# Kernel tuning notes

Measured on AMD Instinct MI355X. Metric: run time of the kernel, lower is better.

Reference implementation:

```python
import jax, jax.numpy as jnp
import numpy as np

N_BAND = 5  # module hardcodes self.n = 5 -> keeps |i-j| <= N_BAND-1 = 4


def setup_inputs() -> dict:
    key = jax.random.key(0)
    ks = jax.random.split(key, 6)
    B, L, H = 4, 2048, 1024
    s = 1.0 / np.sqrt(H)
    return {
        "q": jax.random.normal(ks[0], (B, L, H), jnp.float32),
        "k": jax.random.normal(ks[1], (B, L, H), jnp.float32),
        "Wq": jax.random.normal(ks[2], (H, H), jnp.float32) * s,
        "bq": jax.random.normal(ks[3], (H,), jnp.float32) * s,
        "Wk": jax.random.normal(ks[4], (H, H), jnp.float32) * s,
        "bk": jax.random.normal(ks[5], (H,), jnp.float32) * s,
    }


def reference(q, k, Wq, bq, Wk, bk):
    b, l, e = q.shape
    # nn.Linear: y = x @ W^T + b
    qs = jnp.einsum("ble,he->blh", q, Wq) + bq
    ks = jnp.einsum("ble,he->blh", k, Wk) + bk
    # dense QK^T logits, [b, l, l]
    logits = jnp.einsum("blh,bmh->blm", qs, ks)
    # banded mask: the torch loop zeroes offsets 0..n-1 on both sides -> |i-j| <= n-1
    idx = jnp.arange(l)
    band = jnp.abs(idx[:, None] - idx[None, :]) <= (N_BAND - 1)  # [l, l]
    neg_inf = jnp.array(-jnp.inf, dtype=logits.dtype)
    logits = jnp.where(band[None, :, :], logits, neg_inf)
    # every row contains its diagonal, so softmax is well-defined
    return jax.nn.softmax(logits, axis=-1)
```

## Files before the change

kernel.cpp:

```cpp
#include <hip/hip_runtime.h>
#include <math.h>

#define LSEQ 2048
#define HDIM 1024
#define BATCH 4
#define ROWS (BATCH * LSEQ)
#define NBAND 9

typedef __attribute__((ext_vector_type(8))) short bf16x8;
typedef __attribute__((ext_vector_type(4))) float f32x4;
typedef __attribute__((ext_vector_type(8))) unsigned short u16x8;

#define AS3 __attribute__((address_space(3)))
#define AS1 __attribute__((address_space(1)))

__device__ __forceinline__ void gload16(const void* gp, void* lp) {
    __builtin_amdgcn_global_load_lds((AS1 const unsigned*)gp, (AS3 unsigned*)lp, 16, 0, 0);
}

__device__ __forceinline__ unsigned short f2bf(float x) {
    unsigned u = __float_as_uint(x);
    u += 0x7FFFu + ((u >> 16) & 1u);
    return (unsigned short)(u >> 16);
}
__device__ __forceinline__ float bf2f(unsigned short h) {
    return __uint_as_float(((unsigned)h) << 16);
}

__device__ __forceinline__ void split8(float4 a, float4 b, bf16x8& hi, bf16x8& lo) {
    float v[8] = {a.x, a.y, a.z, a.w, b.x, b.y, b.z, b.w};
#pragma unroll
    for (int j = 0; j < 8; j++) {
        unsigned short h = f2bf(v[j]);
        hi[j] = (short)h;
        lo[j] = (short)f2bf(v[j] - bf2f(h));
    }
}

__global__ __launch_bounds__(256) void wpart_kernel(const float* __restrict__ Wk,
                                                    const float* __restrict__ bq,
                                                    float* __restrict__ wpart) {
    const int b = blockIdx.x;
    const int c0 = threadIdx.x * 4;
    float4 acc = {0.f, 0.f, 0.f, 0.f};
#pragma unroll
    for (int hh = 0; hh < 16; hh++) {
        const int h = b * 16 + hh;
        const float s = bq[h];
        float4 v = *reinterpret_cast<const float4*>(&Wk[(size_t)h * HDIM + c0]);
        acc.x += v.x * s; acc.y += v.y * s; acc.z += v.z * s; acc.w += v.w * s;
    }
    *reinterpret_cast<float4*>(&wpart[(size_t)b * HDIM + c0]) = acc;
}

__global__ __launch_bounds__(256) void wreduce(const float* __restrict__ wpart,
                                               float* __restrict__ w) {
    const int c = blockIdx.x * 256 + threadIdx.x;
    float s = 0.f;
#pragma unroll
    for (int b = 0; b < 64; b++) s += wpart[(size_t)b * HDIM + c];
    w[c] = s;
}

__global__ __launch_bounds__(256) void transpose_convert(const float* __restrict__ Wq,
                                                         const float* __restrict__ Wk,
                                                         unsigned short* __restrict__ qhi,
                                                         unsigned short* __restrict__ qlo,
                                                         unsigned short* __restrict__ khi,
                                                         unsigned short* __restrict__ klo) {
    __shared__ float tile[64][65];
    const int z = blockIdx.z;
    const float* src = z ? Wk : Wq;
    unsigned short* dh = z ? khi : qhi;
    unsigned short* dl = z ? klo : qlo;
    const int n0 = blockIdx.x * 64;
    const int h0 = blockIdx.y * 64;
    const int tid = threadIdx.x;

#pragma unroll
    for (int p = 0; p < 4; p++) {
        const int h = p * 16 + (tid >> 4);
        const int n = (tid & 15) * 4;
        float4 v = *reinterpret_cast<const float4*>(&src[(size_t)(h0 + h) * HDIM + n0 + n]);
        tile[h][n + 0] = v.x; tile[h][n + 1] = v.y; tile[h][n + 2] = v.z; tile[h][n + 3] = v.w;
    }
    __syncthreads();
#pragma unroll
    for (int p = 0; p < 2; p++) {
        const int n = p * 32 + (tid >> 3);
        const int h = (tid & 7) * 8;
        u16x8 hv, lv;
#pragma unroll
        for (int j = 0; j < 8; j++) {
            float x = tile[h + j][n];
            unsigned short hb = f2bf(x);
            hv[j] = hb;
            lv[j] = f2bf(x - bf2f(hb));
        }
        *reinterpret_cast<u16x8*>(&dh[(size_t)(n0 + n) * HDIM + h0 + h]) = hv;
        *reinterpret_cast<u16x8*>(&dl[(size_t)(n0 + n) * HDIM + h0 + h]) = lv;
    }
}

__global__ __launch_bounds__(256) void convert_k_beta(const float* __restrict__ k,
                                                      const float* __restrict__ w,
                                                      unsigned short* __restrict__ Xhi,
                                                      unsigned short* __restrict__ Xlo,
                                                      float* __restrict__ beta) {
    __shared__ float red[4];
    const int r = blockIdx.x;
    const int t = threadIdx.x;
    float4 v = *reinterpret_cast<const float4*>(&k[(size_t)r * HDIM + t * 4]);
    float4 wv = *reinterpret_cast<const float4*>(&w[t * 4]);
    ushort4 h, l;
    h.x = f2bf(v.x); l.x = f2bf(v.x - bf2f(h.x));
    h.y = f2bf(v.y); l.y = f2bf(v.y - bf2f(h.y));
    h.z = f2bf(v.z); l.z = f2bf(v.z - bf2f(h.z));
    h.w = f2bf(v.w); l.w = f2bf(v.w - bf2f(h.w));
    reinterpret_cast<ushort4*>(Xhi)[(size_t)r * 256 + t] = h;
    reinterpret_cast<ushort4*>(Xlo)[(size_t)r * 256 + t] = l;
    float d = v.x * wv.x + v.y * wv.y + v.z * wv.z + v.w * wv.w;
#pragma unroll
    for (int off = 32; off > 0; off >>= 1) d += __shfl_xor(d, off, 64);
    if ((t & 63) == 0) red[t >> 6] = d;
    __syncthreads();
    if (t == 0) beta[r] = red[0] + red[1] + red[2] + red[3];
}

__global__ __launch_bounds__(256, 2) void gemm_part(
        const unsigned short* __restrict__ Ahi, const unsigned short* __restrict__ Alo,
        const unsigned short* __restrict__ Bhi, const unsigned short* __restrict__ Blo,
        float* __restrict__ Cparts) {
    __shared__ unsigned short sh[4 * 4096];
    const int AHI = 0, ALO = 4096, BHI = 8192, BLO = 12288;
    const int tid = threadIdx.x;
    const int w = tid >> 6, l = tid & 63;
    const int wr = w >> 1, wc = w & 1;
    const int row0 = blockIdx.x * 128, col0 = blockIdx.y * 128;
    const int kbeg = blockIdx.z * 256;
    float* C = Cparts + (size_t)blockIdx.z * HDIM * HDIM;
    const int srow0 = (l >> 2), scbp = l & 3;

    f32x4 acc[4][4];
#pragma unroll
    for (int m = 0; m < 4; m++)
#pragma unroll
        for (int n = 0; n < 4; n++) acc[m][n] = (f32x4){0.f, 0.f, 0.f, 0.f};

    const int fr_a[4] = {wr * 64 + (l & 15), wr * 64 + 16 + (l & 15),
                         wr * 64 + 32 + (l & 15), wr * 64 + 48 + (l & 15)};
    const int fr_b[4] = {wc * 64 + (l & 15), wc * 64 + 16 + (l & 15),
                         wc * 64 + 32 + (l & 15), wc * 64 + 48 + (l & 15)};
    const int cb = l >> 4;

    for (int k0 = kbeg; k0 < kbeg + 256; k0 += 32) {
#pragma unroll
        for (int i = 0; i < 2; i++) {
            const int seg = i * 4 + w;
            const int row = seg * 16 + srow0;
            const int cbs = scbp ^ ((row >> 1) & 3);
            gload16(Ahi + (size_t)(row0 + row) * HDIM + k0 + cbs * 8, &sh[AHI + seg * 512]);
            gload16(Alo + (size_t)(row0 + row) * HDIM + k0 + cbs * 8, &sh[ALO + seg * 512]);
            gload16(Bhi + (size_t)(col0 + row) * HDIM + k0 + cbs * 8, &sh[BHI + seg * 512]);
            gload16(Blo + (size_t)(col0 + row) * HDIM + k0 + cbs * 8, &sh[BLO + seg * 512]);
        }
        __syncthreads();

        bf16x8 ah[4], al[4], bh[4], bl[4];
#pragma unroll
        for (int m = 0; m < 4; m++) {
            const int r = fr_a[m];
            const int cbs = cb ^ ((r >> 1) & 3);
            ah[m] = *reinterpret_cast<const bf16x8*>(&sh[AHI + r * 32 + cbs * 8]);
            al[m] = *reinterpret_cast<const bf16x8*>(&sh[ALO + r * 32 + cbs * 8]);
        }
#pragma unroll
        for (int n = 0; n < 4; n++) {
            const int r = fr_b[n];
            const int cbs = cb ^ ((r >> 1) & 3);
            bh[n] = *reinterpret_cast<const bf16x8*>(&sh[BHI + r * 32 + cbs * 8]);
            bl[n] = *reinterpret_cast<const bf16x8*>(&sh[BLO + r * 32 + cbs * 8]);
        }
#pragma unroll
        for (int m = 0; m < 4; m++)
#pragma unroll
            for (int n = 0; n < 4; n++) {
                acc[m][n] = __builtin_amdgcn_mfma_f32_16x16x32_bf16(ah[m], bh[n], acc[m][n], 0, 0, 0);
                acc[m][n] = __builtin_amdgcn_mfma_f32_16x16x32_bf16(ah[m], bl[n], acc[m][n], 0, 0, 0);
                acc[m][n] = __builtin_amdgcn_mfma_f32_16x16x32_bf16(al[m], bh[n], acc[m][n], 0, 0, 0);
            }
        __syncthreads();
    }

    const int lcol = l & 15, lrow = (l >> 4) * 4;
#pragma unroll
    for (int n = 0; n < 4; n++) {
        const int colg = col0 + wc * 64 + n * 16 + lcol;
#pragma unroll
        for (int m = 0; m < 4; m++) {
            const int rowg = row0 + wr * 64 + m * 16 + lrow;
#pragma unroll
            for (int v = 0; v < 4; v++)
                C[(size_t)(rowg + v) * HDIM + colg] = acc[m][n][v];
        }
    }
}

__global__ __launch_bounds__(256) void reduceM_convert(const float* __restrict__ Mparts,
                                                       unsigned short* __restrict__ Mhi,
                                                       unsigned short* __restrict__ Mlo) {
    const int idx4 = blockIdx.x * 256 + threadIdx.x;
    float4 s = {0.f, 0.f, 0.f, 0.f};
#pragma unroll
    for (int z = 0; z < 4; z++) {
        float4 v = reinterpret_cast<const float4*>(Mparts + (size_t)z * HDIM * HDIM)[idx4];
        s.x += v.x; s.y += v.y; s.z += v.z; s.w += v.w;
    }
    ushort4 h, l;
    h.x = f2bf(s.x); l.x = f2bf(s.x - bf2f(h.x));
    h.y = f2bf(s.y); l.y = f2bf(s.y - bf2f(h.y));
    h.z = f2bf(s.z); l.z = f2bf(s.z - bf2f(h.z));
    h.w = f2bf(s.w); l.w = f2bf(s.w - bf2f(h.w));
    reinterpret_cast<ushort4*>(Mhi)[idx4] = h;
    reinterpret_cast<ushort4*>(Mlo)[idx4] = l;
}

__global__ __launch_bounds__(256, 2) void gemm_t(
        const unsigned short* __restrict__ Ahi, const unsigned short* __restrict__ Alo,
        const unsigned short* __restrict__ Bhi, const unsigned short* __restrict__ Blo,
        float* __restrict__ C) {
    __shared__ unsigned short sh[4 * 4096];
    const int AHI = 0, ALO = 4096, BHI = 8192, BLO = 12288;
    const int tid = threadIdx.x;
    const int w = tid >> 6, l = tid & 63;
    const int wr = w >> 1, wc = w & 1;

    const int bid = blockIdx.y * gridDim.x + blockIdx.x;
    const int swz = (bid & 7) * 64 + (bid >> 3);
    const int row0 = (swz & 63) * 128;
    const int col0 = (swz >> 6) * 128;
    const int srow0 = (l >> 2), scbp = l & 3;

    f32x4 acc[4][4];
#pragma unroll
    for (int m = 0; m < 4; m++)
#pragma unroll
        for (int n = 0; n < 4; n++) acc[m][n] = (f32x4){0.f, 0.f, 0.f, 0.f};

    const int fr_a[4] = {wr * 64 + (l & 15), wr * 64 + 16 + (l & 15),
                         wr * 64 + 32 + (l & 15), wr * 64 + 48 + (l & 15)};
    const int fr_b[4] = {wc * 64 + (l & 15), wc * 64 + 16 + (l & 15),
                         wc * 64 + 32 + (l & 15), wc * 64 + 48 + (l & 15)};
    const int cb = l >> 4;

    for (int k0 = 0; k0 < HDIM; k0 += 32) {
#pragma unroll
        for (int i = 0; i < 2; i++) {
            const int seg = i * 4 + w;
            const int row = seg * 16 + srow0;
            const int cbs = scbp ^ ((row >> 1) & 3);
            gload16(Ahi + (size_t)(row0 + row) * HDIM + k0 + cbs * 8, &sh[AHI + seg * 512]);
            gload16(Alo + (size_t)(row0 + row) * HDIM + k0 + cbs * 8, &sh[ALO + seg * 512]);
            gload16(Bhi + (size_t)(col0 + row) * HDIM + k0 + cbs * 8, &sh[BHI + seg * 512]);
            gload16(Blo + (size_t)(col0 + row) * HDIM + k0 + cbs * 8, &sh[BLO + seg * 512]);
        }
        __syncthreads();

        bf16x8 ah[4], al[4], bh[4], bl[4];
#pragma unroll
        for (int m = 0; m < 4; m++) {
            const int r = fr_a[m];
            const int cbs = cb ^ ((r >> 1) & 3);
            ah[m] = *reinterpret_cast<const bf16x8*>(&sh[AHI + r * 32 + cbs * 8]);
            al[m] = *reinterpret_cast<const bf16x8*>(&sh[ALO + r * 32 + cbs * 8]);
        }
#pragma unroll
        for (int n = 0; n < 4; n++) {
            const int r = fr_b[n];
            const int cbs = cb ^ ((r >> 1) & 3);
            bh[n] = *reinterpret_cast<const bf16x8*>(&sh[BHI + r * 32 + cbs * 8]);
            bl[n] = *reinterpret_cast<const bf16x8*>(&sh[BLO + r * 32 + cbs * 8]);
        }
#pragma unroll
        for (int m = 0; m < 4; m++)
#pragma unroll
            for (int n = 0; n < 4; n++) {
                acc[m][n] = __builtin_amdgcn_mfma_f32_16x16x32_bf16(ah[m], bh[n], acc[m][n], 0, 0, 0);
                acc[m][n] = __builtin_amdgcn_mfma_f32_16x16x32_bf16(ah[m], bl[n], acc[m][n], 0, 0, 0);
                acc[m][n] = __builtin_amdgcn_mfma_f32_16x16x32_bf16(al[m], bh[n], acc[m][n], 0, 0, 0);
            }
        __syncthreads();
    }

    const int lcol = l & 15, lrow = (l >> 4) * 4;
#pragma unroll
    for (int n = 0; n < 4; n++) {
        const int colg = col0 + wc * 64 + n * 16 + lcol;
#pragma unroll
        for (int m = 0; m < 4; m++) {
            const int rowg = row0 + wr * 64 + m * 16 + lrow;
#pragma unroll
            for (int v = 0; v < 4; v++)
                C[(size_t)(rowg + v) * HDIM + colg] = acc[m][n][v];
        }
    }
}

__global__ __launch_bounds__(256) void band_mfma(const float* __restrict__ q,
                                                 const float* __restrict__ t,
                                                 const float* __restrict__ beta,
                                                 float* __restrict__ band) {
    __shared__ float lds_c[4][16][33];
    const int tid = threadIdx.x;
    const int w = tid >> 6, l = tid & 63;
    const int r0 = blockIdx.x * 16;
    const int b = r0 >> 11;
    const int i0 = r0 & (LSEQ - 1);
    const int fr = l & 15;
    const int kb = (l >> 4) * 8;

    const float* qrow = q + (size_t)(r0 + fr) * HDIM;
    const float* tbase = t + (size_t)b * LSEQ * HDIM;

    const int j0 = i0 - 4 + fr;
    const int j1 = i0 + 12 + fr;
    const int j0c = min(max(j0, 0), LSEQ - 1);
    const int j1c = min(max(j1, 0), LSEQ - 1);
    const bool v0 = (j0 >= 0) && (j0 < LSEQ);
    const bool v1 = (j1 >= 0) && (j1 < LSEQ);
    const bool interior = (i0 >= 4) && (i0 + 19 < LSEQ);
    const float4 fz = {0.f, 0.f, 0.f, 0.f};

    f32x4 c0 = {0.f, 0.f, 0.f, 0.f};
    f32x4 c1 = {0.f, 0.f, 0.f, 0.f};

#pragma unroll 2
    for (int ks = 0; ks < 8; ks++) {
        const int k0 = w * 256 + ks * 32 + kb;
        float4 qa = *reinterpret_cast<const float4*>(qrow + k0);
        float4 qb = *reinterpret_cast<const float4*>(qrow + k0 + 4);
        float4 t0a = *reinterpret_cast<const float4*>(tbase + (size_t)j0c * HDIM + k0);
        float4 t0b = *reinterpret_cast<const float4*>(tbase + (size_t)j0c * HDIM + k0 + 4);
        float4 t1a = *reinterpret_cast<const float4*>(tbase + (size_t)j1c * HDIM + k0);
        float4 t1b = *reinterpret_cast<const float4*>(tbase + (size_t)j1c * HDIM + k0 + 4);
        if (!interior) {
            if (!v0) { t0a = fz; t0b = fz; }
            if (!v1) { t1a = fz; t1b = fz; }
        }
        bf16x8 ah, al, b0h, b0l, b1h, b1l;
        split8(qa, qb, ah, al);
        split8(t0a, t0b, b0h, b0l);
        split8(t1a, t1b, b1h, b1l);
        c0 = __builtin_amdgcn_mfma_f32_16x16x32_bf16(ah, b0h, c0, 0, 0, 0);
        c0 = __builtin_amdgcn_mfma_f32_16x16x32_bf16(ah, b0l, c0, 0, 0, 0);
        c0 = __builtin_amdgcn_mfma_f32_16x16x32_bf16(al, b0h, c0, 0, 0, 0);
        c1 = __builtin_amdgcn_mfma_f32_16x16x32_bf16(ah, b1h, c1, 0, 0, 0);
        c1 = __builtin_amdgcn_mfma_f32_16x16x32_bf16(ah, b1l, c1, 0, 0, 0);
        c1 = __builtin_amdgcn_mfma_f32_16x16x32_bf16(al, b1h, c1, 0, 0, 0);
    }

#pragma unroll
    for (int v = 0; v < 4; v++) {
        lds_c[w][(l >> 4) * 4 + v][fr] = c0[v];
        lds_c[w][(l >> 4) * 4 + v][16 + fr] = c1[v];
    }
    __syncthreads();

#pragma unroll
    for (int e = tid; e < 512; e += 256) {
        const int rr = e >> 5, cc = e & 31;
        lds_c[0][rr][cc] = lds_c[0][rr][cc] + lds_c[1][rr][cc] +
                           lds_c[2][rr][cc] + lds_c[3][rr][cc];
    }
    __syncthreads();

    if (tid < 16) {
        const int il = i0 + tid;
        const int ig = r0 + tid;
        float lg[NBAND];
#pragma unroll
        for (int d = 0; d < NBAND; d++) {
            const int j = il + d - 4;
            lg[d] = (j >= 0 && j < LSEQ)
                    ? lds_c[0][tid][tid + d] + beta[(size_t)b * LSEQ + j]
                    : -1e30f;
        }
        float m = -1e30f;
#pragma unroll
        for (int d = 0; d < NBAND; d++) m = fmaxf(m, lg[d]);
        float p[NBAND], s = 0.f;
#pragma unroll
        for (int d = 0; d < NBAND; d++) { p[d] = expf(lg[d] - m); s += p[d]; }
        const float inv = 1.f / s;
#pragma unroll
        for (int d = 0; d < NBAND; d++) band[(size_t)ig * NBAND + d] = p[d] * inv;
    }
}

__global__ __launch_bounds__(256) void expand_band(const float* __restrict__ band,
                                                   float* __restrict__ out) {
    const size_t idx4 = (size_t)blockIdx.x * 256 + threadIdx.x;
    const size_t flat = idx4 * 4;
    const int j0 = (int)(flat & (LSEQ - 1));
    const size_t row = flat >> 11;
    const int i = (int)(row & (LSEQ - 1));
    float v[4];
#pragma unroll
    for (int s = 0; s < 4; s++) {
        const int dj = (j0 + s) - i + 4;
        v[s] = (dj >= 0 && dj < NBAND) ? band[row * NBAND + dj] : 0.f;
    }
    float4 o = {v[0], v[1], v[2], v[3]};
    *reinterpret_cast<float4*>(&out[flat]) = o;
}

__global__ __launch_bounds__(256) void gemm_nt_bias(const float* __restrict__ A,
                                                    const float* __restrict__ B,
                                                    const float* __restrict__ bias,
                                                    float* __restrict__ C) {
    __shared__ float As[8][132];
    __shared__ float Bs[8][132];
    const int tid = threadIdx.x;
    const int row0 = blockIdx.x * 128, col0 = blockIdx.y * 128;
    const int lr = tid >> 1, lc = (tid & 1) * 4;
    const int tx = tid & 15, ty = tid >> 4;
    float acc[2][2][4][4];
#pragma unroll
    for (int a = 0; a < 2; a++)
#pragma unroll
        for (int b = 0; b < 2; b++)
#pragma unroll
            for (int c = 0; c < 4; c++)
#pragma unroll
                for (int d = 0; d < 4; d++) acc[a][b][c][d] = 0.f;
    for (int k0 = 0; k0 < HDIM; k0 += 8) {
        float4 av = *reinterpret_cast<const float4*>(&A[(size_t)(row0 + lr) * HDIM + k0 + lc]);
        float4 bv = *reinterpret_cast<const float4*>(&B[(size_t)(col0 + lr) * HDIM + k0 + lc]);
        __syncthreads();
        As[lc + 0][lr] = av.x; As[lc + 1][lr] = av.y; As[lc + 2][lr] = av.z; As[lc + 3][lr] = av.w;
        Bs[lc + 0][lr] = bv.x; Bs[lc + 1][lr] = bv.y; Bs[lc + 2][lr] = bv.z; Bs[lc + 3][lr] = bv.w;
        __syncthreads();
#pragma unroll
        for (int kk = 0; kk < 8; kk++) {
            float4 a0 = *reinterpret_cast<const float4*>(&As[kk][ty * 4]);
            float4 a1 = *reinterpret_cast<const float4*>(&As[kk][64 + ty * 4]);
            float4 b0 = *reinterpret_cast<const float4*>(&Bs[kk][tx * 4]);
            float4 b1 = *reinterpret_cast<const float4*>(&Bs[kk][64 + tx * 4]);
            float am[2][4] = {{a0.x, a0.y, a0.z, a0.w}, {a1.x, a1.y, a1.z, a1.w}};
            float bw[2][4] = {{b0.x, b0.y, b0.z, b0.w}, {b1.x, b1.y, b1.z, b1.w}};
#pragma unroll
            for (int mi = 0; mi < 2; mi++)
#pragma unroll
                for (int ni = 0; ni < 2; ni++)
#pragma unroll
                    for (int mm = 0; mm < 4; mm++)
#pragma unroll
                        for (int nn = 0; nn < 4; nn++)
                            acc[mi][ni][mm][nn] += am[mi][mm] * bw[ni][nn];
        }
    }
#pragma unroll
    for (int mi = 0; mi < 2; mi++)
#pragma unroll
        for (int mm = 0; mm < 4; mm++) {
            const int r = row0 + mi * 64 + ty * 4 + mm;
#pragma unroll
            for (int ni = 0; ni < 2; ni++) {
                const int c = col0 + ni * 64 + tx * 4;
                float4 o;
                o.x = acc[mi][ni][mm][0] + bias[c + 0];
                o.y = acc[mi][ni][mm][1] + bias[c + 1];
                o.z = acc[mi][ni][mm][2] + bias[c + 2];
                o.w = acc[mi][ni][mm][3] + bias[c + 3];
                *reinterpret_cast<float4*>(&C[(size_t)r * HDIM + c]) = o;
            }
        }
}

__global__ __launch_bounds__(256) void band_softmax(const float* __restrict__ qs,
                                                    const float* __restrict__ ks,
                                                    float* __restrict__ band) {
    const int wave = threadIdx.x >> 6;
    const int lane = threadIdx.x & 63;
    const int r = blockIdx.x * 4 + wave;
    const int b = r >> 11;
    const int i = r & (LSEQ - 1);
    const float* qrow = qs + (size_t)r * HDIM;
    const float* kbase = ks + (size_t)b * LSEQ * HDIM;
    float acc[NBAND];
#pragma unroll
    for (int d = 0; d < NBAND; d++) acc[d] = 0.f;
    for (int h = lane; h < HDIM; h += 64) {
        const float qv = qrow[h];
#pragma unroll
        for (int d = 0; d < NBAND; d++) {
            const int j = i + d - 4;
            if (j >= 0 && j < LSEQ)
                acc[d] += qv * kbase[(size_t)j * HDIM + h];
        }
    }
#pragma unroll
    for (int d = 0; d < NBAND; d++) {
        float v = acc[d];
#pragma unroll
        for (int off = 32; off > 0; off >>= 1) v += __shfl_xor(v, off, 64);
        acc[d] = v;
    }
    if (lane == 0) {
        float m = -1e30f;
#pragma unroll
        for (int d = 0; d < NBAND; d++) {
            const int j = i + d - 4;
            if (j >= 0 && j < LSEQ) m = fmaxf(m, acc[d]);
        }
        float p[NBAND];
        float s = 0.f;
#pragma unroll
        for (int d = 0; d < NBAND; d++) {
            const int j = i + d - 4;
            p[d] = (j >= 0 && j < LSEQ) ? expf(acc[d] - m) : 0.f;
            s += p[d];
        }
        const float inv = 1.f / s;
#pragma unroll
        for (int d = 0; d < NBAND; d++) band[(size_t)r * NBAND + d] = p[d] * inv;
    }
}

extern "C" void kernel_launch(void* const* d_in, const int* in_sizes, int n_in,
                              void* d_out, int out_size, void* d_ws, size_t ws_size,
                              hipStream_t stream) {
    const float* q  = (const float*)d_in[0];
    const float* k  = (const float*)d_in[1];
    const float* Wq = (const float*)d_in[2];
    const float* bq = (const float*)d_in[3];
    const float* Wk = (const float*)d_in[4];
    const float* bk = (const float*)d_in[5];
    float* out = (float*)d_out;

    const size_t bandB = (size_t)ROWS * NBAND * sizeof(float);
    char* p = (char*)d_ws;
    float* band = (float*)p;                 p += bandB;
    unsigned short* Xhi = (unsigned short*)p; p += (size_t)ROWS * HDIM * 2;
    unsigned short* Xlo = (unsigned short*)p; p += (size_t)ROWS * HDIM * 2;
    unsigned short* Mhi = (unsigned short*)p; p += (size_t)HDIM * HDIM * 2;
    unsigned short* Mlo = (unsigned short*)p; p += (size_t)HDIM * HDIM * 2;
    float* w        = (float*)p;             p += HDIM * sizeof(float);
    float* wpart    = (float*)p;             p += 64 * HDIM * sizeof(float);
    float* beta     = (float*)p;             p += ROWS * sizeof(float);
    const size_t need = (size_t)(p - (char*)d_ws);

    unsigned short* WqTh = Xhi;
    unsigned short* WqTl = Xhi + (size_t)HDIM * HDIM;
    unsigned short* WkTh = Xhi + 2 * (size_t)HDIM * HDIM;
    unsigned short* WkTl = Xhi + 3 * (size_t)HDIM * HDIM;

    float* t = out;
    float* Mparts = out + (size_t)ROWS * HDIM;

    if (ws_size >= need) {
        wpart_kernel<<<64, 256, 0, stream>>>(Wk, bq, wpart);
        wreduce<<<4, 256, 0, stream>>>(wpart, w);
        dim3 tg(16, 16, 2);
        transpose_convert<<<tg, 256, 0, stream>>>(Wq, Wk, WqTh, WqTl, WkTh, WkTl);
        dim3 mg(8, 8, 4);
        gemm_part<<<mg, 256, 0, stream>>>(WqTh, WqTl, WkTh, WkTl, Mparts);
        reduceM_convert<<<HDIM * HDIM / 4 / 256, 256, 0, stream>>>(Mparts, Mhi, Mlo);
        convert_k_beta<<<ROWS, 256, 0, stream>>>(k, w, Xhi, Xlo, beta);
        dim3 gg(ROWS / 128, HDIM / 128);
        gemm_t<<<gg, 256, 0, stream>>>(Xhi, Xlo, Mhi, Mlo, t);
        band_mfma<<<ROWS / 16, 256, 0, stream>>>(q, t, beta, band);
        expand_band<<<(size_t)ROWS * LSEQ / 4 / 256, 256, 0, stream>>>(band, out);
    } else {
        float* qs = out;
        float* ks = out + (size_t)ROWS * HDIM;
        dim3 gg(ROWS / 128, HDIM / 128);
        gemm_nt_bias<<<gg, 256, 0, stream>>>(q, Wq, bq, qs);
        gemm_nt_bias<<<gg, 256, 0, stream>>>(k, Wk, bk, ks);
        band_softmax<<<ROWS / 4, 256, 0, stream>>>(qs, ks, band);
        expand_band<<<(size_t)ROWS * LSEQ / 4 / 256, 256, 0, stream>>>(band, out);
    }
}
```

Before: 143.6 us.

## Double-buffer LDS in split-bf16 GEMM and drop block index swizzle

Splits the GEMM's shared memory into two 32 KB buffers so the global-to-LDS loads for the next K-step are issued before computing on the current one, with one barrier per iteration instead of two. This is meant to hide global load latency behind the MFMA work. It doubles LDS use per block, which may lower occupancy from the requested two blocks per CU, and it replaces the grouped block-index swizzle with a plain row/column mapping, which can change L2 reuse.

After: 139.3 us. -3.0%, faster.

```diff
diff --git a/kernel.cpp b/kernel.cpp
--- a/kernel.cpp
+++ b/kernel.cpp
@@ -229,16 +229,12 @@
         const unsigned short* __restrict__ Ahi, const unsigned short* __restrict__ Alo,
         const unsigned short* __restrict__ Bhi, const unsigned short* __restrict__ Blo,
         float* __restrict__ C) {
-    __shared__ unsigned short sh[4 * 4096];
+    __shared__ unsigned short sh[2][16384];
     const int AHI = 0, ALO = 4096, BHI = 8192, BLO = 12288;
     const int tid = threadIdx.x;
     const int w = tid >> 6, l = tid & 63;
     const int wr = w >> 1, wc = w & 1;
-
-    const int bid = blockIdx.y * gridDim.x + blockIdx.x;
-    const int swz = (bid & 7) * 64 + (bid >> 3);
-    const int row0 = (swz & 63) * 128;
-    const int col0 = (swz >> 6) * 128;
+    const int row0 = blockIdx.x * 128, col0 = blockIdx.y * 128;
     const int srow0 = (l >> 2), scbp = l & 3;
 
     f32x4 acc[4][4];
@@ -253,33 +249,33 @@
                          wc * 64 + 32 + (l & 15), wc * 64 + 48 + (l & 15)};
     const int cb = l >> 4;
 
-    for (int k0 = 0; k0 < HDIM; k0 += 32) {
+    auto stage = [&](int buf, int k0) {
 #pragma unroll
         for (int i = 0; i < 2; i++) {
             const int seg = i * 4 + w;
             const int row = seg * 16 + srow0;
             const int cbs = scbp ^ ((row >> 1) & 3);
-            gload16(Ahi + (size_t)(row0 + row) * HDIM + k0 + cbs * 8, &sh[AHI + seg * 512]);
-            gload16(Alo + (size_t)(row0 + row) * HDIM + k0 + cbs * 8, &sh[ALO + seg * 512]);
-            gload16(Bhi + (size_t)(col0 + row) * HDIM + k0 + cbs * 8, &sh[BHI + seg * 512]);
-            gload16(Blo + (size_t)(col0 + row) * HDIM + k0 + cbs * 8, &sh[BLO + seg * 512]);
-        }
-        __syncthreads();
-
+            gload16(Ahi + (size_t)(row0 + row) * HDIM + k0 + cbs * 8, &sh[buf][AHI + seg * 512]);
+            gload16(Alo + (size_t)(row0 + row) * HDIM + k0 + cbs * 8, &sh[buf][ALO + seg * 512]);
+            gload16(Bhi + (size_t)(col0 + row) * HDIM + k0 + cbs * 8, &sh[buf][BHI + seg * 512]);
+            gload16(Blo + (size_t)(col0 + row) * HDIM + k0 + cbs * 8, &sh[buf][BLO + seg * 512]);
+        }
+    };
+    auto compute = [&](int buf) {
         bf16x8 ah[4], al[4], bh[4], bl[4];
 #pragma unroll
         for (int m = 0; m < 4; m++) {
             const int r = fr_a[m];
             const int cbs = cb ^ ((r >> 1) & 3);
-            ah[m] = *reinterpret_cast<const bf16x8*>(&sh[AHI + r * 32 + cbs * 8]);
-            al[m] = *reinterpret_cast<const bf16x8*>(&sh[ALO + r * 32 + cbs * 8]);
+            ah[m] = *reinterpret_cast<const bf16x8*>(&sh[buf][AHI + r * 32 + cbs * 8]);
+            al[m] = *reinterpret_cast<const bf16x8*>(&sh[buf][ALO + r * 32 + cbs * 8]);
         }
 #pragma unroll
         for (int n = 0; n < 4; n++) {
             const int r = fr_b[n];
             const int cbs = cb ^ ((r >> 1) & 3);
-            bh[n] = *reinterpret_cast<const bf16x8*>(&sh[BHI + r * 32 + cbs * 8]);
-            bl[n] = *reinterpret_cast<const bf16x8*>(&sh[BLO + r * 32 + cbs * 8]);
+            bh[n] = *reinterpret_cast<const bf16x8*>(&sh[buf][BHI + r * 32 + cbs * 8]);
+            bl[n] = *reinterpret_cast<const bf16x8*>(&sh[buf][BLO + r * 32 + cbs * 8]);
         }
 #pragma unroll
         for (int m = 0; m < 4; m++)
@@ -289,8 +285,18 @@
                 acc[m][n] = __builtin_amdgcn_mfma_f32_16x16x32_bf16(ah[m], bl[n], acc[m][n], 0, 0, 0);
                 acc[m][n] = __builtin_amdgcn_mfma_f32_16x16x32_bf16(al[m], bh[n], acc[m][n], 0, 0, 0);
             }
+    };
+
+    stage(0, 0);
+    __syncthreads();
+    int cur = 0;
+    for (int t = 0; t < 31; t++) {
+        stage(cur ^ 1, (t + 1) * 32);
+        compute(cur);
         __syncthreads();
-    }
+        cur ^= 1;
+    }
+    compute(cur);
 
     const int lcol = l & 15, lrow = (l >> 4) * 4;
 #pragma unroll
```
